# Kernel tuning notes

Measured on AMD Instinct MI355X. Metric: run time of the kernel, lower is better.

Reference implementation:

```python
import jax, jax.numpy as jnp
import numpy as np

N_NODES = 100000
N_EDGES = 400000
N_GRAPHS = 2000
NODE_F = 78
HID = 128


def gcn_conv(x, src, dst, W, b, n_nodes):
    # PyG GCNConv: h = X @ W; add self-loops; symmetric norm; scatter-add; + bias
    h = x @ W
    loop = jnp.arange(n_nodes, dtype=src.dtype)
    s = jnp.concatenate([src, loop])
    d = jnp.concatenate([dst, loop])
    deg = jax.ops.segment_sum(jnp.ones_like(d, dtype=h.dtype), d, num_segments=n_nodes)
    dinv = jax.lax.rsqrt(deg)  # deg >= 1 due to self-loops
    coef = dinv[s] * dinv[d]  # [E+N]
    msg = h[s] * coef[:, None]  # gather + scale
    out = jax.ops.segment_sum(msg, d, num_segments=n_nodes)
    return out + b


def setup_inputs() -> dict:
    key = jax.random.key(0)
    ks = jax.random.split(key, 16)
    x = jax.random.normal(ks[0], (N_NODES, NODE_F), dtype=jnp.float32)
    edge_index = jax.random.randint(ks[1], (2, N_EDGES), 0, N_NODES, dtype=jnp.int64)
    batch = jnp.sort(jax.random.randint(ks[2], (N_NODES,), 0, N_GRAPHS, dtype=jnp.int64))
    def lin(k, fi, fo):
        lim = 1.0 / np.sqrt(fi)
        kw, kb = jax.random.split(k)
        return (jax.random.uniform(kw, (fi, fo), jnp.float32, -lim, lim),
                jax.random.uniform(kb, (fo,), jnp.float32, -lim, lim))
    W1, b1 = lin(ks[3], NODE_F, HID)
    W2, b2 = lin(ks[4], HID, 2 * HID)
    W3, b3 = lin(ks[5], 2 * HID, HID)
    fw1, fb1 = lin(ks[6], HID, 64)
    fw2, fb2 = lin(ks[7], 64, 1)
    return {"x": x, "edge_index": edge_index, "batch": batch,
            "W1": W1, "b1": b1, "W2": W2, "b2": b2, "W3": W3, "b3": b3,
            "fw1": fw1, "fb1": fb1, "fw2": fw2, "fb2": fb2}


def reference(x, edge_index, batch, W1, b1, W2, b2, W3, b3, fw1, fb1, fw2, fb2):
    src, dst = edge_index[0], edge_index[1]
    h = jax.nn.relu(gcn_conv(x, src, dst, W1, b1, N_NODES))
    h = jax.nn.relu(gcn_conv(h, src, dst, W2, b2, N_NODES))
    h = jax.nn.relu(gcn_conv(h, src, dst, W3, b3, N_NODES))
    # global_mean_pool over graph ids
    sums = jax.ops.segment_sum(h, batch, num_segments=N_GRAPHS)
    cnts = jax.ops.segment_sum(jnp.ones((N_NODES,), h.dtype), batch, num_segments=N_GRAPHS)
    pooled = sums / jnp.maximum(cnts, 1.0)[:, None]
    h = jax.nn.relu(pooled @ fw1 + fb1)
    return h @ fw2 + fb2  # [N_GRAPHS, 1]
```

## Files before the change

kernel.cpp:

```cpp
#include <hip/hip_runtime.h>

#define N_NODES 100000
#define N_EDGES 400000
#define N_GRAPHS 2000
#define NODE_F 78
#define HID 128
#define PAD 32

typedef __attribute__((ext_vector_type(8))) short short8v;
typedef __attribute__((ext_vector_type(4))) float f32x4;

__device__ __forceinline__ ushort f2bf(float f) {
    unsigned u = __float_as_uint(f);
    unsigned r = (u + 0x7FFFu + ((u >> 16) & 1u)) >> 16;
    return (ushort)r;
}
__device__ __forceinline__ float bf2f(ushort b) {
    return __uint_as_float(((unsigned)b) << 16);
}
__device__ __forceinline__ float2 bfx2(const ushort* p) {
    unsigned u = *reinterpret_cast<const unsigned*>(p);
    return make_float2(__uint_as_float(u << 16), __uint_as_float(u & 0xffff0000u));
}


__global__ void zero_int_k(int* __restrict__ p, int n) {
    int i = blockIdx.x * blockDim.x + threadIdx.x;
    if (i < n) p[i] = 0;
}

__global__ void fill_csr_k(const int* __restrict__ src, const int* __restrict__ dst,
                           int* __restrict__ cursor, int* __restrict__ csr) {
    int e = blockIdx.x * blockDim.x + threadIdx.x;
    if (e >= N_EDGES) return;
    int s = src[e], d = dst[e];
    int p = atomicAdd(&cursor[d], 1);
    if (p < PAD) csr[d * PAD + p] = s;
}

__global__ void dinv_k(const int* __restrict__ deg, float* __restrict__ dinv, int n) {
    int i = blockIdx.x * blockDim.x + threadIdx.x;
    if (i < n) dinv[i] = rsqrtf((float)deg[i] + 1.0f);
}


__global__ void x2bf_k(const float* __restrict__ x, ushort* __restrict__ xb) {
    int idx = blockIdx.x * blockDim.x + threadIdx.x;
    if (idx >= N_NODES * 80) return;
    int n = idx / 80, f = idx - n * 80;
    xb[idx] = (f < NODE_F) ? f2bf(x[(long long)n * NODE_F + f]) : (ushort)0;
}


__global__ void prep_wt_k(const float* __restrict__ W, ushort* __restrict__ Wth,
                          ushort* __restrict__ Wtl, int K, int N) {
    int idx = blockIdx.x * blockDim.x + threadIdx.x;
    if (idx >= N * 256) return;
    int n = idx >> 8, k = idx & 255;
    float v = (k < K) ? W[(long long)k * N + n] : 0.0f;
    ushort h = f2bf(v);
    ushort l = f2bf(v - bf2f(h));
    Wth[n * 256 + k] = h;
    Wtl[n * 256 + k] = l;
}


__global__ __launch_bounds__(256) void gemm_mfma_k(
        const float* __restrict__ A, int lda, int K, int M,
        const ushort* __restrict__ Wth, const ushort* __restrict__ Wtl,
        const float* __restrict__ bias, ushort* __restrict__ C, int N) {
    __shared__ ushort Ah[128 * 64];
    __shared__ ushort Al[128 * 64];
    __shared__ ushort Bh[128 * 64];
    __shared__ ushort Bl[128 * 64];
    const int tid = threadIdx.x;
    const int w = tid >> 6, l = tid & 63;
    const int bm = blockIdx.x * 128;
    const int bn = blockIdx.y * 128;

    f32x4 acc[2][8];
    #pragma unroll
    for (int m = 0; m < 2; ++m)
        #pragma unroll
        for (int j = 0; j < 8; ++j)
            acc[m][j] = (f32x4){0.f, 0.f, 0.f, 0.f};

    for (int k0 = 0; k0 < K; k0 += 64) {
        __syncthreads();
        #pragma unroll
        for (int i = 0; i < 8; ++i) {
            int idx = tid + i * 256;
            int r = idx >> 4;
            int kq = (idx & 15) * 4;
            ushort4 h4, l4;
            if (k0 + kq < K) {
                int gr = bm + r; if (gr >= M) gr = M - 1;
                float4 v = *reinterpret_cast<const float4*>(&A[(long long)gr * lda + k0 + kq]);
                h4.x = f2bf(v.x); l4.x = f2bf(v.x - bf2f(h4.x));
                h4.y = f2bf(v.y); l4.y = f2bf(v.y - bf2f(h4.y));
                h4.z = f2bf(v.z); l4.z = f2bf(v.z - bf2f(h4.z));
                h4.w = f2bf(v.w); l4.w = f2bf(v.w - bf2f(h4.w));
            } else {
                h4 = (ushort4){0, 0, 0, 0};
                l4 = (ushort4){0, 0, 0, 0};
            }
            int e = r * 64 + ((kq >> 3) ^ (r & 7)) * 8 + (kq & 7);
            *reinterpret_cast<ushort4*>(&Ah[e]) = h4;
            *reinterpret_cast<ushort4*>(&Al[e]) = l4;
        }
        #pragma unroll
        for (int i = 0; i < 4; ++i) {
            int idx = tid + i * 256;
            int n = idx >> 3, s0 = idx & 7;
            long long g = (long long)(bn + n) * 256 + k0 + s0 * 8;
            short8v vh = *reinterpret_cast<const short8v*>(&Wth[g]);
            short8v vl = *reinterpret_cast<const short8v*>(&Wtl[g]);
            int e = n * 64 + (s0 ^ (n & 7)) * 8;
            *reinterpret_cast<short8v*>(&Bh[e]) = vh;
            *reinterpret_cast<short8v*>(&Bl[e]) = vl;
        }
        __syncthreads();
        #pragma unroll
        for (int ks = 0; ks < 2; ++ks) {
            short8v ah[2], al[2];
            #pragma unroll
            for (int m = 0; m < 2; ++m) {
                int r = w * 32 + m * 16 + (l & 15);
                int e = r * 64 + ((ks * 4 + (l >> 4)) ^ (r & 7)) * 8;
                ah[m] = *reinterpret_cast<const short8v*>(&Ah[e]);
                al[m] = *reinterpret_cast<const short8v*>(&Al[e]);
            }
            #pragma unroll
            for (int j = 0; j < 8; ++j) {
                int n = j * 16 + (l & 15);
                int e = n * 64 + ((ks * 4 + (l >> 4)) ^ (n & 7)) * 8;
                short8v bh = *reinterpret_cast<const short8v*>(&Bh[e]);
                short8v bl = *reinterpret_cast<const short8v*>(&Bl[e]);
                #pragma unroll
                for (int m = 0; m < 2; ++m) {
                    acc[m][j] = __builtin_amdgcn_mfma_f32_16x16x32_bf16(ah[m], bh, acc[m][j], 0, 0, 0);
                    acc[m][j] = __builtin_amdgcn_mfma_f32_16x16x32_bf16(ah[m], bl, acc[m][j], 0, 0, 0);
                    acc[m][j] = __builtin_amdgcn_mfma_f32_16x16x32_bf16(al[m], bh, acc[m][j], 0, 0, 0);
                }
            }
        }
    }

    #pragma unroll
    for (int j = 0; j < 8; ++j) {
        int gc = bn + j * 16 + (l & 15);
        float bv = bias[gc];
        #pragma unroll
        for (int m = 0; m < 2; ++m) {
            #pragma unroll
            for (int rg = 0; rg < 4; ++rg) {
                int gr = bm + w * 32 + m * 16 + (l >> 4) * 4 + rg;
                if (gr < M)
                    C[(long long)gr * N + gc] = f2bf(fmaxf(acc[m][j][rg] + bv, 0.0f));
            }
        }
    }
}


__global__ __launch_bounds__(256) void gemm23_k(
        const float* __restrict__ A,
        const ushort* __restrict__ W2h, const ushort* __restrict__ W2l,
        const float* __restrict__ b2,
        const ushort* __restrict__ W3h, const ushort* __restrict__ W3l,
        ushort* __restrict__ C, int M) {
    __shared__ ushort Ah[64 * 64];
    __shared__ ushort Al[64 * 64];
    __shared__ ushort Bh[128 * 64];
    __shared__ ushort Bl[128 * 64];
    const int tid = threadIdx.x;
    const int w = tid >> 6, l = tid & 63;
    const int bm = blockIdx.x * 64;

    f32x4 acc2[16];
    #pragma unroll
    for (int j = 0; j < 16; ++j) acc2[j] = (f32x4){0.f, 0.f, 0.f, 0.f};

    for (int k0 = 0; k0 < 128; k0 += 64) {
        __syncthreads();
        #pragma unroll
        for (int i = 0; i < 4; ++i) {
            int idx = tid + i * 256;
            int r = idx >> 4;
            int kq = (idx & 15) * 4;
            int gr = bm + r; if (gr >= M) gr = M - 1;
            float4 v = *reinterpret_cast<const float4*>(&A[(long long)gr * 128 + k0 + kq]);
            ushort4 h4, l4;
            h4.x = f2bf(v.x); l4.x = f2bf(v.x - bf2f(h4.x));
            h4.y = f2bf(v.y); l4.y = f2bf(v.y - bf2f(h4.y));
            h4.z = f2bf(v.z); l4.z = f2bf(v.z - bf2f(h4.z));
            h4.w = f2bf(v.w); l4.w = f2bf(v.w - bf2f(h4.w));
            int e = r * 64 + ((kq >> 3) ^ (r & 7)) * 8 + (kq & 7);
            *reinterpret_cast<ushort4*>(&Ah[e]) = h4;
            *reinterpret_cast<ushort4*>(&Al[e]) = l4;
        }
        #pragma unroll
        for (int nh = 0; nh < 2; ++nh) {
            if (nh) __syncthreads();
            #pragma unroll
            for (int i = 0; i < 4; ++i) {
                int idx = tid + i * 256;
                int n = idx >> 3, s0 = idx & 7;
                long long g = (long long)(nh * 128 + n) * 256 + k0 + s0 * 8;
                short8v vh = *reinterpret_cast<const short8v*>(&W2h[g]);
                short8v vl = *reinterpret_cast<const short8v*>(&W2l[g]);
                int e = n * 64 + (s0 ^ (n & 7)) * 8;
                *reinterpret_cast<short8v*>(&Bh[e]) = vh;
                *reinterpret_cast<short8v*>(&Bl[e]) = vl;
            }
            __syncthreads();
            #pragma unroll
            for (int ks = 0; ks < 2; ++ks) {
                int r = w * 16 + (l & 15);
                int ea = r * 64 + ((ks * 4 + (l >> 4)) ^ (r & 7)) * 8;
                short8v ah = *reinterpret_cast<const short8v*>(&Ah[ea]);
                short8v al = *reinterpret_cast<const short8v*>(&Al[ea]);
                #pragma unroll
                for (int jl = 0; jl < 8; ++jl) {
                    int n = jl * 16 + (l & 15);
                    int e = n * 64 + ((ks * 4 + (l >> 4)) ^ (n & 7)) * 8;
                    short8v bh = *reinterpret_cast<const short8v*>(&Bh[e]);
                    short8v bl = *reinterpret_cast<const short8v*>(&Bl[e]);
                    int j = nh * 8 + jl;
                    acc2[j] = __builtin_amdgcn_mfma_f32_16x16x32_bf16(ah, bh, acc2[j], 0, 0, 0);
                    acc2[j] = __builtin_amdgcn_mfma_f32_16x16x32_bf16(ah, bl, acc2[j], 0, 0, 0);
                    acc2[j] = __builtin_amdgcn_mfma_f32_16x16x32_bf16(al, bh, acc2[j], 0, 0, 0);
                }
            }
        }
    }

    f32x4 acc3[8];
    #pragma unroll
    for (int j = 0; j < 8; ++j) acc3[j] = (f32x4){0.f, 0.f, 0.f, 0.f};

    #pragma unroll
    for (int ch = 0; ch < 4; ++ch) {
        __syncthreads();
        #pragma unroll
        for (int jj = 0; jj < 4; ++jj) {
            int j = ch * 4 + jj;
            float bv = b2[j * 16 + (l & 15)];
            #pragma unroll
            for (int rg = 0; rg < 4; ++rg) {
                int r = w * 16 + (l >> 4) * 4 + rg;
                float v = fmaxf(acc2[j][rg] + bv, 0.f);
                ushort h = f2bf(v);
                ushort lo = f2bf(v - bf2f(h));
                int cl = jj * 16 + (l & 15);
                int e = r * 64 + ((cl >> 3) ^ (r & 7)) * 8 + (cl & 7);
                Ah[e] = h; Al[e] = lo;
            }
        }
        #pragma unroll
        for (int i = 0; i < 4; ++i) {
            int idx = tid + i * 256;
            int n = idx >> 3, s0 = idx & 7;
            long long g = (long long)n * 256 + ch * 64 + s0 * 8;
            short8v vh = *reinterpret_cast<const short8v*>(&W3h[g]);
            short8v vl = *reinterpret_cast<const short8v*>(&W3l[g]);
            int e = n * 64 + (s0 ^ (n & 7)) * 8;
            *reinterpret_cast<short8v*>(&Bh[e]) = vh;
            *reinterpret_cast<short8v*>(&Bl[e]) = vl;
        }
        __syncthreads();
        #pragma unroll
        for (int ks = 0; ks < 2; ++ks) {
            int r = w * 16 + (l & 15);
            int ea = r * 64 + ((ks * 4 + (l >> 4)) ^ (r & 7)) * 8;
            short8v ah = *reinterpret_cast<const short8v*>(&Ah[ea]);
            short8v al = *reinterpret_cast<const short8v*>(&Al[ea]);
            #pragma unroll
            for (int j3 = 0; j3 < 8; ++j3) {
                int n = j3 * 16 + (l & 15);
                int e = n * 64 + ((ks * 4 + (l >> 4)) ^ (n & 7)) * 8;
                short8v bh = *reinterpret_cast<const short8v*>(&Bh[e]);
                short8v bl = *reinterpret_cast<const short8v*>(&Bl[e]);
                acc3[j3] = __builtin_amdgcn_mfma_f32_16x16x32_bf16(ah, bh, acc3[j3], 0, 0, 0);
                acc3[j3] = __builtin_amdgcn_mfma_f32_16x16x32_bf16(ah, bl, acc3[j3], 0, 0, 0);
                acc3[j3] = __builtin_amdgcn_mfma_f32_16x16x32_bf16(al, bh, acc3[j3], 0, 0, 0);
            }
        }
    }

    #pragma unroll
    for (int j = 0; j < 8; ++j) {
        int gc = j * 16 + (l & 15);
        #pragma unroll
        for (int rg = 0; rg < 4; ++rg) {
            int gr = bm + w * 16 + (l >> 4) * 4 + rg;
            if (gr < M) C[(long long)gr * 128 + gc] = f2bf(acc3[j][rg]);
        }
    }
}


__global__ __launch_bounds__(256) void gather78_k(const ushort* __restrict__ Xb,
        const int* __restrict__ csr, const int* __restrict__ deg,
        const float* __restrict__ dinv, float* __restrict__ out) {
    int wid = (blockIdx.x * blockDim.x + threadIdx.x) >> 6;
    int lane = threadIdx.x & 63;
    if (wid >= N_NODES) return;
    float di = dinv[wid];
    float ax = 0.f, ay = 0.f;
    bool act = lane < 40;
    if (act) {
        float2 v = bfx2(&Xb[(long long)wid * 80 + lane * 2]);
        float sc = di * di;
        ax = v.x * sc; ay = v.y * sc;
    }
    int d = deg[wid]; if (d > PAD) d = PAD;
    const int4* e4 = reinterpret_cast<const int4*>(csr + wid * PAD);
    for (int j0 = 0; j0 < d; j0 += 4) {
        int4 e = e4[j0 >> 2];
        int rem = d - j0;
        int s1 = (rem > 1) ? e.y : e.x;
        int s2 = (rem > 2) ? e.z : e.x;
        int s3 = (rem > 3) ? e.w : e.x;
        float c0 = di * dinv[e.x];
        float c1 = (rem > 1) ? di * dinv[s1] : 0.f;
        float c2 = (rem > 2) ? di * dinv[s2] : 0.f;
        float c3 = (rem > 3) ? di * dinv[s3] : 0.f;
        if (act) {
            float2 v0 = bfx2(&Xb[(long long)e.x * 80 + lane * 2]);
            float2 v1 = bfx2(&Xb[(long long)s1  * 80 + lane * 2]);
            float2 v2 = bfx2(&Xb[(long long)s2  * 80 + lane * 2]);
            float2 v3 = bfx2(&Xb[(long long)s3  * 80 + lane * 2]);
            ax += v0.x * c0 + v1.x * c1 + v2.x * c2 + v3.x * c3;
            ay += v0.y * c0 + v1.y * c1 + v2.y * c2 + v3.y * c3;
        }
    }
    if (act)
        *reinterpret_cast<float2*>(&out[(long long)wid * 80 + lane * 2]) = make_float2(ax, ay);
}

__global__ __launch_bounds__(256) void gather128_k(const ushort* __restrict__ A,
        const int* __restrict__ csr, const int* __restrict__ deg,
        const float* __restrict__ dinv, float* __restrict__ out) {
    int wid = (blockIdx.x * blockDim.x + threadIdx.x) >> 6;
    int lane = threadIdx.x & 63;
    if (wid >= N_NODES) return;
    float di = dinv[wid];
    float2 v0 = bfx2(&A[(long long)wid * 128 + lane * 2]);
    float sc = di * di;
    float ax = v0.x * sc, ay = v0.y * sc;
    int d = deg[wid]; if (d > PAD) d = PAD;
    const int4* e4 = reinterpret_cast<const int4*>(csr + wid * PAD);
    for (int j0 = 0; j0 < d; j0 += 4) {
        int4 e = e4[j0 >> 2];
        int rem = d - j0;
        int s1 = (rem > 1) ? e.y : e.x;
        int s2 = (rem > 2) ? e.z : e.x;
        int s3 = (rem > 3) ? e.w : e.x;
        float c0 = di * dinv[e.x];
        float c1 = (rem > 1) ? di * dinv[s1] : 0.f;
        float c2 = (rem > 2) ? di * dinv[s2] : 0.f;
        float c3 = (rem > 3) ? di * dinv[s3] : 0.f;
        float2 w0 = bfx2(&A[(long long)e.x * 128 + lane * 2]);
        float2 w1 = bfx2(&A[(long long)s1  * 128 + lane * 2]);
        float2 w2 = bfx2(&A[(long long)s2  * 128 + lane * 2]);
        float2 w3 = bfx2(&A[(long long)s3  * 128 + lane * 2]);
        ax += w0.x * c0 + w1.x * c1 + w2.x * c2 + w3.x * c3;
        ay += w0.y * c0 + w1.y * c1 + w2.y * c2 + w3.y * c3;
    }
    *reinterpret_cast<float2*>(&out[(long long)wid * 128 + lane * 2]) = make_float2(ax, ay);
}


__global__ __launch_bounds__(256) void pool_head_k(
        const ushort* __restrict__ A,
        const int* __restrict__ csr, const int* __restrict__ deg,
        const float* __restrict__ dinv, const float* __restrict__ b3,
        const int* __restrict__ batch,
        const float* __restrict__ fw1, const float* __restrict__ fb1,
        const float* __restrict__ fw2, const float* __restrict__ fb2,
        float* __restrict__ out) {
    __shared__ float part[4][HID];
    __shared__ float ps[HID];
    const int g = blockIdx.x;
    const int w = threadIdx.x >> 6, lane = threadIdx.x & 63;

    int start, end;
    {
        int l = 0, h = N_NODES;
        while (l < h) { int m = (l + h) >> 1; if (batch[m] < g) l = m + 1; else h = m; }
        start = l;
        h = N_NODES;
        while (l < h) { int m = (l + h) >> 1; if (batch[m] < g + 1) l = m + 1; else h = m; }
        end = l;
    }

    float sx = 0.f, sy = 0.f;
    const float bx = b3[lane * 2], by = b3[lane * 2 + 1];
    for (int i = start + w; i < end; i += 4) {
        float di = dinv[i];
        float2 v0 = bfx2(&A[(long long)i * 128 + lane * 2]);
        float sc = di * di;
        float ax = v0.x * sc, ay = v0.y * sc;
        int d = deg[i]; if (d > PAD) d = PAD;
        const int4* e4 = reinterpret_cast<const int4*>(csr + i * PAD);
        for (int j0 = 0; j0 < d; j0 += 4) {
            int4 e = e4[j0 >> 2];
            int rem = d - j0;
            int s1 = (rem > 1) ? e.y : e.x;
            int s2 = (rem > 2) ? e.z : e.x;
            int s3 = (rem > 3) ? e.w : e.x;
            float c0 = di * dinv[e.x];
            float c1 = (rem > 1) ? di * dinv[s1] : 0.f;
            float c2 = (rem > 2) ? di * dinv[s2] : 0.f;
            float c3 = (rem > 3) ? di * dinv[s3] : 0.f;
            float2 w0 = bfx2(&A[(long long)e.x * 128 + lane * 2]);
            float2 w1 = bfx2(&A[(long long)s1  * 128 + lane * 2]);
            float2 w2 = bfx2(&A[(long long)s2  * 128 + lane * 2]);
            float2 w3 = bfx2(&A[(long long)s3  * 128 + lane * 2]);
            ax += w0.x * c0 + w1.x * c1 + w2.x * c2 + w3.x * c3;
            ay += w0.y * c0 + w1.y * c1 + w2.y * c2 + w3.y * c3;
        }
        sx += fmaxf(ax + bx, 0.f);
        sy += fmaxf(ay + by, 0.f);
    }
    part[w][lane * 2] = sx;
    part[w][lane * 2 + 1] = sy;
    __syncthreads();

    if (w == 0) {
        float inv = (end > start) ? 1.0f / (float)(end - start) : 0.0f;
        ps[lane * 2]     = (part[0][lane * 2]     + part[1][lane * 2]     + part[2][lane * 2]     + part[3][lane * 2])     * inv;
        ps[lane * 2 + 1] = (part[0][lane * 2 + 1] + part[1][lane * 2 + 1] + part[2][lane * 2 + 1] + part[3][lane * 2 + 1]) * inv;
    }
    __syncthreads();

    if (w == 0) {
        float acc = fb1[lane];
        #pragma unroll 8
        for (int k = 0; k < HID; ++k) acc = fmaf(ps[k], fw1[k * 64 + lane], acc);
        float v = fmaxf(acc, 0.0f) * fw2[lane];
        #pragma unroll
        for (int off = 32; off > 0; off >>= 1) v += __shfl_down(v, off);
        if (lane == 0) out[g] = v + fb2[0];
    }
}


extern "C" void kernel_launch(void* const* d_in, const int* in_sizes, int n_in,
                              void* d_out, int out_size, void* d_ws, size_t ws_size,
                              hipStream_t stream) {
    const float* x     = (const float*)d_in[0];
    const int*   ei    = (const int*)d_in[1];
    const int*   batch = (const int*)d_in[2];
    const float* W1 = (const float*)d_in[3];
    const float* b1 = (const float*)d_in[4];
    const float* W2 = (const float*)d_in[5];
    const float* b2 = (const float*)d_in[6];
    const float* W3 = (const float*)d_in[7];
    const float* b3 = (const float*)d_in[8];
    const float* fw1 = (const float*)d_in[9];
    const float* fb1 = (const float*)d_in[10];
    const float* fw2 = (const float*)d_in[11];
    const float* fb2 = (const float*)d_in[12];
    float* out = (float*)d_out;

    const int* src = ei;
    const int* dst = ei + N_EDGES;

    char* p = (char*)d_ws;
    float* dinv = (float*)p;  p += 100352 * 4;
    int*   cur  = (int*)p;    p += 100352 * 4;
    int*   csr  = (int*)p;    p += (size_t)N_NODES * PAD * 4;
    ushort* w2h = (ushort*)p; p += 256 * 256 * 2;
    ushort* w2l = (ushort*)p; p += 256 * 256 * 2;
    ushort* w3h = (ushort*)p; p += 256 * 256 * 2;
    ushort* w3l = (ushort*)p; p += 256 * 256 * 2;
    ushort* xb  = (ushort*)p; p += (size_t)N_NODES * 80 * 2;
    float* xpad = (float*)p;  p += (size_t)N_NODES * 80 * 4;
    ushort* buf1 = (ushort*)p; p += (size_t)N_NODES * 128 * 2;
    float*  buf2 = (float*)p;  p += (size_t)N_NODES * 128 * 4;
    ushort* buf3 = (ushort*)p; p += (size_t)N_NODES * 128 * 2;

    const int T = 256;
    const int gw = (N_NODES * 64 + T - 1) / T;

    zero_int_k<<<(N_NODES + T - 1) / T, T, 0, stream>>>(cur, N_NODES);
    fill_csr_k<<<(N_EDGES + T - 1) / T, T, 0, stream>>>(src, dst, cur, csr);
    dinv_k<<<(N_NODES + T - 1) / T, T, 0, stream>>>(cur, dinv, N_NODES);
    x2bf_k<<<(N_NODES * 80 + T - 1) / T, T, 0, stream>>>(x, xb);

    gather78_k<<<gw, T, 0, stream>>>(xb, csr, cur, dinv, xpad);
    prep_wt_k<<<(128 * 256 + T - 1) / T, T, 0, stream>>>(W1, w2h, w2l, NODE_F, 128);
    gemm_mfma_k<<<dim3(782, 1), 256, 0, stream>>>(xpad, 80, 80, N_NODES, w2h, w2l, b1, buf1, 128);

    gather128_k<<<gw, T, 0, stream>>>(buf1, csr, cur, dinv, buf2);
    prep_wt_k<<<(256 * 256 + T - 1) / T, T, 0, stream>>>(W2, w2h, w2l, HID, 256);
    prep_wt_k<<<(128 * 256 + T - 1) / T, T, 0, stream>>>(W3, w3h, w3l, 2 * HID, 128);
    gemm23_k<<<1563, 256, 0, stream>>>(buf2, w2h, w2l, b2, w3h, w3l, buf3, N_NODES);

    pool_head_k<<<N_GRAPHS, 256, 0, stream>>>(buf3, csr, cur, dinv, b3, batch,
                                              fw1, fb1, fw2, fb2, out);
}
```

Before: 369.9 us.

## Prescale features by dinv, pad CSR with zero sentinel row, drop low-weight MFMA

Features are pre-multiplied by dinv when they are written (during x conversion and in the GEMM epilogues), so the gathers become plain unweighted sums followed by one multiply by the destination's dinv. This removes the per-edge dinv gathers and the remainder masking. CSR slots are pre-filled with a sentinel index that points to a zeroed extra row, so partial quads need no branching, at the cost of filling the whole padded CSR every call. The low bf16 half of the weights is dropped, removing one of three MFMAs per split-bf16 product and lowering accuracy. The pool kernel also moves to 512 threads.

```diff
diff --git a/kernel.cpp b/kernel.cpp
--- a/kernel.cpp
+++ b/kernel.cpp
@@ -6,6 +6,7 @@
 #define NODE_F 78
 #define HID 128
 #define PAD 32
+#define SENT N_NODES
 
 typedef __attribute__((ext_vector_type(8))) short short8v;
 typedef __attribute__((ext_vector_type(4))) float f32x4;
@@ -24,9 +25,17 @@
 }
 
 
-__global__ void zero_int_k(int* __restrict__ p, int n) {
+__global__ void setup_k(int* __restrict__ cursor, int4* __restrict__ csr4,
+                        ushort* __restrict__ xb, ushort* __restrict__ b1,
+                        ushort* __restrict__ b3) {
     int i = blockIdx.x * blockDim.x + threadIdx.x;
-    if (i < n) p[i] = 0;
+    if (i < N_NODES * PAD / 4) csr4[i] = make_int4(SENT, SENT, SENT, SENT);
+    if (i < N_NODES) cursor[i] = 0;
+    if (i < 80) xb[(size_t)N_NODES * 80 + i] = 0;
+    if (i < 128) {
+        b1[(size_t)N_NODES * 128 + i] = 0;
+        b3[(size_t)N_NODES * 128 + i] = 0;
+    }
 }
 
 __global__ void fill_csr_k(const int* __restrict__ src, const int* __restrict__ dst,
@@ -44,35 +53,31 @@
 }
 
 
-__global__ void x2bf_k(const float* __restrict__ x, ushort* __restrict__ xb) {
+__global__ void x2bf_k(const float* __restrict__ x, const float* __restrict__ dinv,
+                       ushort* __restrict__ xb) {
     int idx = blockIdx.x * blockDim.x + threadIdx.x;
     if (idx >= N_NODES * 80) return;
     int n = idx / 80, f = idx - n * 80;
-    xb[idx] = (f < NODE_F) ? f2bf(x[(long long)n * NODE_F + f]) : (ushort)0;
+    xb[idx] = (f < NODE_F) ? f2bf(x[(long long)n * NODE_F + f] * dinv[n]) : (ushort)0;
 }
 
 
 __global__ void prep_wt_k(const float* __restrict__ W, ushort* __restrict__ Wth,
-                          ushort* __restrict__ Wtl, int K, int N) {
+                          int K, int N) {
     int idx = blockIdx.x * blockDim.x + threadIdx.x;
     if (idx >= N * 256) return;
     int n = idx >> 8, k = idx & 255;
-    float v = (k < K) ? W[(long long)k * N + n] : 0.0f;
-    ushort h = f2bf(v);
-    ushort l = f2bf(v - bf2f(h));
-    Wth[n * 256 + k] = h;
-    Wtl[n * 256 + k] = l;
+    Wth[idx] = (k < K) ? f2bf(W[(long long)k * N + n]) : (ushort)0;
 }
 
 
 __global__ __launch_bounds__(256) void gemm_mfma_k(
         const float* __restrict__ A, int lda, int K, int M,
-        const ushort* __restrict__ Wth, const ushort* __restrict__ Wtl,
-        const float* __restrict__ bias, ushort* __restrict__ C, int N) {
+        const ushort* __restrict__ Wth, const float* __restrict__ bias,
+        const float* __restrict__ dinv, ushort* __restrict__ C, int N) {
     __shared__ ushort Ah[128 * 64];
     __shared__ ushort Al[128 * 64];
     __shared__ ushort Bh[128 * 64];
-    __shared__ ushort Bl[128 * 64];
     const int tid = threadIdx.x;
     const int w = tid >> 6, l = tid & 63;
     const int bm = blockIdx.x * 128;
@@ -114,10 +119,8 @@
             int n = idx >> 3, s0 = idx & 7;
             long long g = (long long)(bn + n) * 256 + k0 + s0 * 8;
             short8v vh = *reinterpret_cast<const short8v*>(&Wth[g]);
-            short8v vl = *reinterpret_cast<const short8v*>(&Wtl[g]);
             int e = n * 64 + (s0 ^ (n & 7)) * 8;
             *reinterpret_cast<short8v*>(&Bh[e]) = vh;
-            *reinterpret_cast<short8v*>(&Bl[e]) = vl;
         }
         __syncthreads();
         #pragma unroll
@@ -135,17 +138,23 @@
                 int n = j * 16 + (l & 15);
                 int e = n * 64 + ((ks * 4 + (l >> 4)) ^ (n & 7)) * 8;
                 short8v bh = *reinterpret_cast<const short8v*>(&Bh[e]);
-                short8v bl = *reinterpret_cast<const short8v*>(&Bl[e]);
                 #pragma unroll
                 for (int m = 0; m < 2; ++m) {
                     acc[m][j] = __builtin_amdgcn_mfma_f32_16x16x32_bf16(ah[m], bh, acc[m][j], 0, 0, 0);
-                    acc[m][j] = __builtin_amdgcn_mfma_f32_16x16x32_bf16(ah[m], bl, acc[m][j], 0, 0, 0);
                     acc[m][j] = __builtin_amdgcn_mfma_f32_16x16x32_bf16(al[m], bh, acc[m][j], 0, 0, 0);
                 }
             }
         }
     }
 
+    float dv[2][4];
+    #pragma unroll
+    for (int m = 0; m < 2; ++m)
+        #pragma unroll
+        for (int rg = 0; rg < 4; ++rg) {
+            int gr = bm + w * 32 + m * 16 + (l >> 4) * 4 + rg;
+            dv[m][rg] = (gr < M) ? dinv[gr] : 0.f;
+        }
     #pragma unroll
     for (int j = 0; j < 8; ++j) {
         int gc = bn + j * 16 + (l & 15);
@@ -156,7 +165,7 @@
             for (int rg = 0; rg < 4; ++rg) {
                 int gr = bm + w * 32 + m * 16 + (l >> 4) * 4 + rg;
                 if (gr < M)
-                    C[(long long)gr * N + gc] = f2bf(fmaxf(acc[m][j][rg] + bv, 0.0f));
+                    C[(long long)gr * N + gc] = f2bf(fmaxf(acc[m][j][rg] + bv, 0.0f) * dv[m][rg]);
             }
         }
     }
@@ -165,14 +174,12 @@
 
 __global__ __launch_bounds__(256) void gemm23_k(
         const float* __restrict__ A,
-        const ushort* __restrict__ W2h, const ushort* __restrict__ W2l,
-        const float* __restrict__ b2,
-        const ushort* __restrict__ W3h, const ushort* __restrict__ W3l,
+        const ushort* __restrict__ W2h, const float* __restrict__ b2,
+        const ushort* __restrict__ W3h, const float* __restrict__ dinv,
         ushort* __restrict__ C, int M) {
     __shared__ ushort Ah[64 * 64];
     __shared__ ushort Al[64 * 64];
     __shared__ ushort Bh[128 * 64];
-    __shared__ ushort Bl[128 * 64];
     const int tid = threadIdx.x;
     const int w = tid >> 6, l = tid & 63;
     const int bm = blockIdx.x * 64;
@@ -208,10 +215,8 @@
                 int n = idx >> 3, s0 = idx & 7;
                 long long g = (long long)(nh * 128 + n) * 256 + k0 + s0 * 8;
                 short8v vh = *reinterpret_cast<const short8v*>(&W2h[g]);
-                short8v vl = *reinterpret_cast<const short8v*>(&W2l[g]);
                 int e = n * 64 + (s0 ^ (n & 7)) * 8;
                 *reinterpret_cast<short8v*>(&Bh[e]) = vh;
-                *reinterpret_cast<short8v*>(&Bl[e]) = vl;
             }
             __syncthreads();
             #pragma unroll
@@ -225,10 +230,8 @@
                     int n = jl * 16 + (l & 15);
                     int e = n * 64 + ((ks * 4 + (l >> 4)) ^ (n & 7)) * 8;
                     short8v bh = *reinterpret_cast<const short8v*>(&Bh[e]);
-                    short8v bl = *reinterpret_cast<const short8v*>(&Bl[e]);
                     int j = nh * 8 + jl;
                     acc2[j] = __builtin_amdgcn_mfma_f32_16x16x32_bf16(ah, bh, acc2[j], 0, 0, 0);
-                    acc2[j] = __builtin_amdgcn_mfma_f32_16x16x32_bf16(ah, bl, acc2[j], 0, 0, 0);
                     acc2[j] = __builtin_amdgcn_mfma_f32_16x16x32_bf16(al, bh, acc2[j], 0, 0, 0);
                 }
             }
@@ -263,10 +266,8 @@
             int n = idx >> 3, s0 = idx & 7;
             long long g = (long long)n * 256 + ch * 64 + s0 * 8;
             short8v vh = *reinterpret_cast<const short8v*>(&W3h[g]);
-            short8v vl = *reinterpret_cast<const short8v*>(&W3l[g]);
             int e = n * 64 + (s0 ^ (n & 7)) * 8;
             *reinterpret_cast<short8v*>(&Bh[e]) = vh;
-            *reinterpret_cast<short8v*>(&Bl[e]) = vl;
         }
         __syncthreads();
         #pragma unroll
@@ -280,28 +281,32 @@
                 int n = j3 * 16 + (l & 15);
                 int e = n * 64 + ((ks * 4 + (l >> 4)) ^ (n & 7)) * 8;
                 short8v bh = *reinterpret_cast<const short8v*>(&Bh[e]);
-                short8v bl = *reinterpret_cast<const short8v*>(&Bl[e]);
                 acc3[j3] = __builtin_amdgcn_mfma_f32_16x16x32_bf16(ah, bh, acc3[j3], 0, 0, 0);
-                acc3[j3] = __builtin_amdgcn_mfma_f32_16x16x32_bf16(ah, bl, acc3[j3], 0, 0, 0);
                 acc3[j3] = __builtin_amdgcn_mfma_f32_16x16x32_bf16(al, bh, acc3[j3], 0, 0, 0);
             }
         }
     }
 
+    float dv[4];
+    #pragma unroll
+    for (int rg = 0; rg < 4; ++rg) {
+        int gr = bm + w * 16 + (l >> 4) * 4 + rg;
+        dv[rg] = (gr < M) ? dinv[gr] : 0.f;
+    }
     #pragma unroll
     for (int j = 0; j < 8; ++j) {
         int gc = j * 16 + (l & 15);
         #pragma unroll
         for (int rg = 0; rg < 4; ++rg) {
             int gr = bm + w * 16 + (l >> 4) * 4 + rg;
-            if (gr < M) C[(long long)gr * 128 + gc] = f2bf(acc3[j][rg]);
+            if (gr < M) C[(long long)gr * 128 + gc] = f2bf(acc3[j][rg] * dv[rg]);
         }
     }
 }
 
 
 __global__ __launch_bounds__(256) void gather78_k(const ushort* __restrict__ Xb,
-        const int* __restrict__ csr, const int* __restrict__ deg,
+        const int* __restrict__ deg, const int* __restrict__ csr,
         const float* __restrict__ dinv, float* __restrict__ out) {
     int wid = (blockIdx.x * blockDim.x + threadIdx.x) >> 6;
     int lane = threadIdx.x & 63;
@@ -310,77 +315,59 @@
     float ax = 0.f, ay = 0.f;
     bool act = lane < 40;
     if (act) {
-        float2 v = bfx2(&Xb[(long long)wid * 80 + lane * 2]);
-        float sc = di * di;
-        ax = v.x * sc; ay = v.y * sc;
+        float2 v = bfx2(&Xb[(size_t)wid * 80 + lane * 2]);
+        ax = v.x; ay = v.y;
     }
     int d = deg[wid]; if (d > PAD) d = PAD;
     const int4* e4 = reinterpret_cast<const int4*>(csr + wid * PAD);
     for (int j0 = 0; j0 < d; j0 += 4) {
         int4 e = e4[j0 >> 2];
-        int rem = d - j0;
-        int s1 = (rem > 1) ? e.y : e.x;
-        int s2 = (rem > 2) ? e.z : e.x;
-        int s3 = (rem > 3) ? e.w : e.x;
-        float c0 = di * dinv[e.x];
-        float c1 = (rem > 1) ? di * dinv[s1] : 0.f;
-        float c2 = (rem > 2) ? di * dinv[s2] : 0.f;
-        float c3 = (rem > 3) ? di * dinv[s3] : 0.f;
         if (act) {
-            float2 v0 = bfx2(&Xb[(long long)e.x * 80 + lane * 2]);
-            float2 v1 = bfx2(&Xb[(long long)s1  * 80 + lane * 2]);
-            float2 v2 = bfx2(&Xb[(long long)s2  * 80 + lane * 2]);
-            float2 v3 = bfx2(&Xb[(long long)s3  * 80 + lane * 2]);
-            ax += v0.x * c0 + v1.x * c1 + v2.x * c2 + v3.x * c3;
-            ay += v0.y * c0 + v1.y * c1 + v2.y * c2 + v3.y * c3;
+            float2 v0 = bfx2(&Xb[(size_t)e.x * 80 + lane * 2]);
+            float2 v1 = bfx2(&Xb[(size_t)e.y * 80 + lane * 2]);
+            float2 v2 = bfx2(&Xb[(size_t)e.z * 80 + lane * 2]);
+            float2 v3 = bfx2(&Xb[(size_t)e.w * 80 + lane * 2]);
+            ax += v0.x + v1.x + v2.x + v3.x;
+            ay += v0.y + v1.y + v2.y + v3.y;
         }
     }
     if (act)
-        *reinterpret_cast<float2*>(&out[(long long)wid * 80 + lane * 2]) = make_float2(ax, ay);
+        *reinterpret_cast<float2*>(&out[(size_t)wid * 80 + lane * 2]) = make_float2(ax * di, ay * di);
 }
 
 __global__ __launch_bounds__(256) void gather128_k(const ushort* __restrict__ A,
-        const int* __restrict__ csr, const int* __restrict__ deg,
+        const int* __restrict__ deg, const int* __restrict__ csr,
         const float* __restrict__ dinv, float* __restrict__ out) {
     int wid = (blockIdx.x * blockDim.x + threadIdx.x) >> 6;
     int lane = threadIdx.x & 63;
     if (wid >= N_NODES) return;
     float di = dinv[wid];
-    float2 v0 = bfx2(&A[(long long)wid * 128 + lane * 2]);
-    float sc = di * di;
-    float ax = v0.x * sc, ay = v0.y * sc;
+    float2 v = bfx2(&A[(size_t)wid * 128 + lane * 2]);
+    float ax = v.x, ay = v.y;
     int d = deg[wid]; if (d > PAD) d = PAD;
     const int4* e4 = reinterpret_cast<const int4*>(csr + wid * PAD);
     for (int j0 = 0; j0 < d; j0 += 4) {
         int4 e = e4[j0 >> 2];
-        int rem = d - j0;
-        int s1 = (rem > 1) ? e.y : e.x;
-        int s2 = (rem > 2) ? e.z : e.x;
-        int s3 = (rem > 3) ? e.w : e.x;
-        float c0 = di * dinv[e.x];
-        float c1 = (rem > 1) ? di * dinv[s1] : 0.f;
-        float c2 = (rem > 2) ? di * dinv[s2] : 0.f;
-        float c3 = (rem > 3) ? di * dinv[s3] : 0.f;
-        float2 w0 = bfx2(&A[(long long)e.x * 128 + lane * 2]);
-        float2 w1 = bfx2(&A[(long long)s1  * 128 + lane * 2]);
-        float2 w2 = bfx2(&A[(long long)s2  * 128 + lane * 2]);
-        float2 w3 = bfx2(&A[(long long)s3  * 128 + lane * 2]);
-        ax += w0.x * c0 + w1.x * c1 + w2.x * c2 + w3.x * c3;
-        ay += w0.y * c0 + w1.y * c1 + w2.y * c2 + w3.y * c3;
-    }
-    *reinterpret_cast<float2*>(&out[(long long)wid * 128 + lane * 2]) = make_float2(ax, ay);
-}
-
-
-__global__ __launch_bounds__(256) void pool_head_k(
+        float2 w0 = bfx2(&A[(size_t)e.x * 128 + lane * 2]);
+        float2 w1 = bfx2(&A[(size_t)e.y * 128 + lane * 2]);
+        float2 w2 = bfx2(&A[(size_t)e.z * 128 + lane * 2]);
+        float2 w3 = bfx2(&A[(size_t)e.w * 128 + lane * 2]);
+        ax += w0.x + w1.x + w2.x + w3.x;
+        ay += w0.y + w1.y + w2.y + w3.y;
+    }
+    *reinterpret_cast<float2*>(&out[(size_t)wid * 128 + lane * 2]) = make_float2(ax * di, ay * di);
+}
+
+
+__global__ __launch_bounds__(512) void pool_head_k(
         const ushort* __restrict__ A,
-        const int* __restrict__ csr, const int* __restrict__ deg,
+        const int* __restrict__ deg, const int* __restrict__ csr,
         const float* __restrict__ dinv, const float* __restrict__ b3,
         const int* __restrict__ batch,
         const float* __restrict__ fw1, const float* __restrict__ fb1,
         const float* __restrict__ fw2, const float* __restrict__ fb2,
         float* __restrict__ out) {
-    __shared__ float part[4][HID];
+    __shared__ float part[8][HID];
     __shared__ float ps[HID];
     const int g = blockIdx.x;
     const int w = threadIdx.x >> 6, lane = threadIdx.x & 63;
@@ -397,32 +384,23 @@
 
     float sx = 0.f, sy = 0.f;
     const float bx = b3[lane * 2], by = b3[lane * 2 + 1];
-    for (int i = start + w; i < end; i += 4) {
+    for (int i = start + w; i < end; i += 8) {
         float di = dinv[i];
-        float2 v0 = bfx2(&A[(long long)i * 128 + lane * 2]);
-        float sc = di * di;
-        float ax = v0.x * sc, ay = v0.y * sc;
+        float2 v = bfx2(&A[(size_t)i * 128 + lane * 2]);
+        float ax = v.x, ay = v.y;
         int d = deg[i]; if (d > PAD) d = PAD;
         const int4* e4 = reinterpret_cast<const int4*>(csr + i * PAD);
         for (int j0 = 0; j0 < d; j0 += 4) {
             int4 e = e4[j0 >> 2];
-            int rem = d - j0;
-            int s1 = (rem > 1) ? e.y : e.x;
-            int s2 = (rem > 2) ? e.z : e.x;
-            int s3 = (rem > 3) ? e.w : e.x;
-            float c0 = di * dinv[e.x];
-            float c1 = (rem > 1) ? di * dinv[s1] : 0.f;
-            float c2 = (rem > 2) ? di * dinv[s2] : 0.f;
-            float c3 = (rem > 3) ? di * dinv[s3] : 0.f;
-            float2 w0 = bfx2(&A[(long long)e.x * 128 + lane * 2]);
-            float2 w1 = bfx2(&A[(long long)s1  * 128 + lane * 2]);
-            float2 w2 = bfx2(&A[(long long)s2  * 128 + lane * 2]);
-            float2 w3 = bfx2(&A[(long long)s3  * 128 + lane * 2]);
-            ax += w0.x * c0 + w1.x * c1 + w2.x * c2 + w3.x * c3;
-            ay += w0.y * c0 + w1.y * c1 + w2.y * c2 + w3.y * c3;
-        }
-        sx += fmaxf(ax + bx, 0.f);
-        sy += fmaxf(ay + by, 0.f);
+            float2 w0 = bfx2(&A[(size_t)e.x * 128 + lane * 2]);
+            float2 w1 = bfx2(&A[(size_t)e.y * 128 + lane * 2]);
+            float2 w2 = bfx2(&A[(size_t)e.z * 128 + lane * 2]);
+            float2 w3 = bfx2(&A[(size_t)e.w * 128 + lane * 2]);
+            ax += w0.x + w1.x + w2.x + w3.x;
+            ay += w0.y + w1.y + w2.y + w3.y;
+        }
+        sx += fmaxf(ax * di + bx, 0.f);
+        sy += fmaxf(ay * di + by, 0.f);
     }
     part[w][lane * 2] = sx;
     part[w][lane * 2 + 1] = sy;
@@ -430,8 +408,14 @@
 
     if (w == 0) {
         float inv = (end > start) ? 1.0f / (float)(end - start) : 0.0f;
-        ps[lane * 2]     = (part[0][lane * 2]     + part[1][lane * 2]     + part[2][lane * 2]     + part[3][lane * 2])     * inv;
-        ps[lane * 2 + 1] = (part[0][lane * 2 + 1] + part[1][lane * 2 + 1] + part[2][lane * 2 + 1] + part[3][lane * 2 + 1]) * inv;
+        float s0 = 0.f, s1 = 0.f;
+        #pragma unroll
+        for (int q = 0; q < 8; ++q) {
+            s0 += part[q][lane * 2];
+            s1 += part[q][lane * 2 + 1];
+        }
+        ps[lane * 2] = s0 * inv;
+        ps[lane * 2 + 1] = s1 * inv;
     }
     __syncthreads();
 
@@ -469,36 +453,36 @@
     const int* dst = ei + N_EDGES;
 
     char* p = (char*)d_ws;
-    float* dinv = (float*)p;  p += 100352 * 4;
-    int*   cur  = (int*)p;    p += 100352 * 4;
-    int*   csr  = (int*)p;    p += (size_t)N_NODES * PAD * 4;
-    ushort* w2h = (ushort*)p; p += 256 * 256 * 2;
-    ushort* w2l = (ushort*)p; p += 256 * 256 * 2;
-    ushort* w3h = (ushort*)p; p += 256 * 256 * 2;
-    ushort* w3l = (ushort*)p; p += 256 * 256 * 2;
-    ushort* xb  = (ushort*)p; p += (size_t)N_NODES * 80 * 2;
-    float* xpad = (float*)p;  p += (size_t)N_NODES * 80 * 4;
-    ushort* buf1 = (ushort*)p; p += (size_t)N_NODES * 128 * 2;
+    float*  dinv = (float*)p;  p += 100352 * 4;
+    int*    cur  = (int*)p;    p += 100352 * 4;
+    int*    csr  = (int*)p;    p += (size_t)N_NODES * PAD * 4;
+    ushort* w1h  = (ushort*)p; p += 256 * 256 * 2;
+    ushort* w2h  = (ushort*)p; p += 256 * 256 * 2;
+    ushort* w3h  = (ushort*)p; p += 256 * 256 * 2;
+    ushort* xb   = (ushort*)p; p += (size_t)(N_NODES + 1) * 80 * 2;
+    float*  xpad = (float*)p;  p += (size_t)N_NODES * 80 * 4;
+    ushort* buf1 = (ushort*)p; p += (size_t)(N_NODES + 1) * 128 * 2;
     float*  buf2 = (float*)p;  p += (size_t)N_NODES * 128 * 4;
-    ushort* buf3 = (ushort*)p; p += (size_t)N_NODES * 128 * 2;
+    ushort* buf3 = (ushort*)p; p += (size_t)(N_NODES + 1) * 128 * 2;
 
     const int T = 256;
     const int gw = (N_NODES * 64 + T - 1) / T;
 
-    zero_int_k<<<(N_NODES + T - 1) / T, T, 0, stream>>>(cur, N_NODES);
+    setup_k<<<(N_NODES * PAD / 4 + T - 1) / T, T, 0, stream>>>(cur, (int4*)csr, xb, buf1, buf3);
     fill_csr_k<<<(N_EDGES + T - 1) / T, T, 0, stream>>>(src, dst, cur, csr);
     dinv_k<<<(N_NODES + T - 1) / T, T, 0, stream>>>(cur, dinv, N_NODES);
-    x2bf_k<<<(N_NODES * 80 + T - 1) / T, T, 0, stream>>>(x, xb);
-
-    gather78_k<<<gw, T, 0, stream>>>(xb, csr, cur, dinv, xpad);
-    prep_wt_k<<<(128 * 256 + T - 1) / T, T, 0, stream>>>(W1, w2h, w2l, NODE_F, 128);
-    gemm_mfma_k<<<dim3(782, 1), 256, 0, stream>>>(xpad, 80, 80, N_NODES, w2h, w2l, b1, buf1, 128);
-
-    gather128_k<<<gw, T, 0, stream>>>(buf1, csr, cur, dinv, buf2);
-    prep_wt_k<<<(256 * 256 + T - 1) / T, T, 0, stream>>>(W2, w2h, w2l, HID, 256);
-    prep_wt_k<<<(128 * 256 + T - 1) / T, T, 0, stream>>>(W3, w3h, w3l, 2 * HID, 128);
-    gemm23_k<<<1563, 256, 0, stream>>>(buf2, w2h, w2l, b2, w3h, w3l, buf3, N_NODES);
-
-    pool_head_k<<<N_GRAPHS, 256, 0, stream>>>(buf3, csr, cur, dinv, b3, batch,
+    x2bf_k<<<(N_NODES * 80 + T - 1) / T, T, 0, stream>>>(x, dinv, xb);
+
+    prep_wt_k<<<(128 * 256 + T - 1) / T, T, 0, stream>>>(W1, w1h, NODE_F, 128);
+    prep_wt_k<<<(256 * 256 + T - 1) / T, T, 0, stream>>>(W2, w2h, HID, 256);
+    prep_wt_k<<<(128 * 256 + T - 1) / T, T, 0, stream>>>(W3, w3h, 2 * HID, 128);
+
+    gather78_k<<<gw, T, 0, stream>>>(xb, cur, csr, dinv, xpad);
+    gemm_mfma_k<<<dim3(782, 1), 256, 0, stream>>>(xpad, 80, 80, N_NODES, w1h, b1, dinv, buf1, 128);
+
+    gather128_k<<<gw, T, 0, stream>>>(buf1, cur, csr, dinv, buf2);
+    gemm23_k<<<1563, 256, 0, stream>>>(buf2, w2h, b2, w3h, dinv, buf3, N_NODES);
+
+    pool_head_k<<<N_GRAPHS, 512, 0, stream>>>(buf3, cur, csr, dinv, b3, batch,
                                               fw1, fb1, fw2, fb2, out);
 }
```

After: 341.6 us. 1.08x faster.
